# Kernel optimization log

Measured on AMD Instinct MI355X. Metric: run time of the kernel, lower is better.

Reference implementation:

```python
import jax, jax.numpy as jnp
import numpy as np


def setup_inputs() -> dict:
    key = jax.random.key(0)
    k0, k1, k2, k3 = jax.random.split(key, 4)
    B, T, D, F, E = 4, 2048, 512, 1024, 8
    x = jax.random.normal(k0, (B, T, D), dtype=jnp.float32)
    # router weight is zero-init in the original; use small random values so top-k
    router_w = 0.02 * jax.random.normal(k1, (E, D), dtype=jnp.float32)
    router_b = jnp.zeros((E,), dtype=jnp.float32)
    w_gate_up = 0.02 * jax.random.normal(k2, (E, D, 2 * F), dtype=jnp.float32)
    w_down = 0.02 * jax.random.normal(k3, (E, F, D), dtype=jnp.float32)
    return {"x": x, "router_w": router_w, "router_b": router_b,
            "w_gate_up": w_gate_up, "w_down": w_down, "top_k": 2}


def reference(x, router_w, router_b, w_gate_up, w_down, top_k):
    B, T, D = x.shape
    E = router_w.shape[0]
    x_flat = x.reshape(-1, D)                      # [N, D]
    N = x_flat.shape[0]

    # router: softmax over experts, top-k, renormalize
    logits = x_flat @ router_w.T + router_b       # [N, E]
    probs = jax.nn.softmax(logits, axis=-1)
    top_w, top_idx = jax.lax.top_k(probs, top_k)  # [N, k]
    top_w = top_w / jnp.sum(top_w, axis=-1, keepdims=True)

    # scatter renormalized weights into a dense [N, E] combine matrix
    combine = jnp.zeros((N, E), dtype=x.dtype).at[
        jnp.arange(N)[:, None], top_idx].add(top_w)

    # per-expert SwiGLU; combine weights zero out non-selected experts, giving
    # math identical to the sort/gather/scatter dispatch in the original
    out = jnp.zeros_like(x_flat)
    for e in range(E):  # fixed small expert count, not a data-dim loop
        gate_up = x_flat @ w_gate_up[e]           # [N, 2F]
        gate, up = jnp.split(gate_up, 2, axis=-1)
        h = jax.nn.silu(gate) * up                # [N, F]
        out = out + combine[:, e:e + 1] * (h @ w_down[e])
    return out.reshape(B, T, D)
```

## Files before the change

### kernel.cpp

```cpp
#include <hip/hip_runtime.h>
#include <stdint.h>

#define N_TOK 8192
#define D_DIM 512
#define F_DIM 1024
#define E_NUM 8
#define M_SLOTS (N_TOK * 2)
#define NTILE_MAX 136

typedef __bf16 bf16x8 __attribute__((ext_vector_type(8)));
typedef float f32x4 __attribute__((ext_vector_type(4)));

__device__ __forceinline__ ushort f2b(float f) {
    union { float f; unsigned u; } v; v.f = f;
    unsigned r = v.u + 0x7fffu + ((v.u >> 16) & 1u);
    return (ushort)(r >> 16);
}
__device__ __forceinline__ float b2f(ushort u) {
    union { unsigned i; float f; } v; v.i = ((unsigned)u) << 16; return v.f;
}
__device__ __forceinline__ void gload16(const void* g, void* l) {
    __builtin_amdgcn_global_load_lds(
        (const __attribute__((address_space(1))) unsigned int*)g,
        (__attribute__((address_space(3))) unsigned int*)l, 16, 0, 0);
}

__global__ __launch_bounds__(256) void pre_k(const float* __restrict__ x,
                                             const float* __restrict__ rw,
                                             const float* __restrict__ rb,
                                             ushort* __restrict__ x_bf,
                                             int* __restrict__ tok_e,
                                             float* __restrict__ tok_w,
                                             int* __restrict__ cnt,
                                             const float* __restrict__ wgu,
                                             ushort* __restrict__ wgu_t,
                                             const float* __restrict__ wd,
                                             ushort* __restrict__ wd_t) {
    __shared__ ushort tile[64][65];
    int b = blockIdx.x;
    if (b < N_TOK / 4) {
        if (b == 0 && threadIdx.x < 16) cnt[threadIdx.x] = 0;
        int lane = threadIdx.x & 63, wv = threadIdx.x >> 6;
        int t = b * 4 + wv;
        float4 xa = *(const float4*)(x + (size_t)t * D_DIM + lane * 8);
        float4 xb = *(const float4*)(x + (size_t)t * D_DIM + lane * 8 + 4);
        ushort u[8] = {f2b(xa.x), f2b(xa.y), f2b(xa.z), f2b(xa.w),
                       f2b(xb.x), f2b(xb.y), f2b(xb.z), f2b(xb.w)};
        *(uint4*)(x_bf + (size_t)t * D_DIM + lane * 8) = *(const uint4*)u;

        float acc[E_NUM];
#pragma unroll
        for (int e = 0; e < E_NUM; ++e) {
            float4 wa = *(const float4*)(rw + (size_t)e * D_DIM + lane * 8);
            float4 wb = *(const float4*)(rw + (size_t)e * D_DIM + lane * 8 + 4);
            float s = xa.x * wa.x + xa.y * wa.y + xa.z * wa.z + xa.w * wa.w +
                      xb.x * wb.x + xb.y * wb.y + xb.z * wb.z + xb.w * wb.w;
#pragma unroll
            for (int o = 32; o > 0; o >>= 1) s += __shfl_xor(s, o, 64);
            acc[e] = s;
        }
        if (lane == 0) {
            float l[E_NUM];
#pragma unroll
            for (int e = 0; e < E_NUM; ++e) l[e] = acc[e] + rb[e];
            int e0 = 0;
#pragma unroll
            for (int e = 1; e < E_NUM; ++e) if (l[e] > l[e0]) e0 = e;
            int e1 = (e0 == 0) ? 1 : 0;
#pragma unroll
            for (int e = 0; e < E_NUM; ++e) if (e != e0 && l[e] > l[e1]) e1 = e;
            float p1 = __expf(l[e1] - l[e0]);
            float w0 = 1.f / (1.f + p1), w1 = p1 / (1.f + p1);
            tok_e[2 * t] = e0;  tok_e[2 * t + 1] = e1;
            tok_w[2 * t] = w0;  tok_w[2 * t + 1] = w1;
        }
        return;
    }
    int tb = b - N_TOK / 4;
    const float* src; ushort* dst; int R, C, c0, r0;
    if (tb < 2048) {
        int e = tb >> 8, rem = tb & 255;
        R = D_DIM; C = 2 * F_DIM;
        src = wgu + (size_t)e * R * C; dst = wgu_t + (size_t)e * R * C;
        c0 = (rem & 31) * 64; r0 = (rem >> 5) * 64;
    } else {
        int b2 = tb - 2048;
        int e = b2 >> 7, rem = b2 & 127;
        R = F_DIM; C = D_DIM;
        src = wd + (size_t)e * R * C; dst = wd_t + (size_t)e * R * C;
        c0 = (rem & 7) * 64; r0 = (rem >> 3) * 64;
    }
#pragma unroll
    for (int i = 0; i < 4; ++i) {
        int ch = threadIdx.x + i * 256;
        int row = ch >> 4, pos = ch & 15;
        float4 v = *(const float4*)(src + (size_t)(r0 + row) * C + c0 + pos * 4);
        tile[row][pos * 4 + 0] = f2b(v.x);
        tile[row][pos * 4 + 1] = f2b(v.y);
        tile[row][pos * 4 + 2] = f2b(v.z);
        tile[row][pos * 4 + 3] = f2b(v.w);
    }
    __syncthreads();
#pragma unroll
    for (int i = 0; i < 2; ++i) {
        int ch = threadIdx.x + i * 256;
        int ocol = ch >> 3, rb_ = ch & 7;
        ushort tmp[8];
#pragma unroll
        for (int j = 0; j < 8; ++j) tmp[j] = tile[rb_ * 8 + j][ocol];
        *(uint4*)(dst + (size_t)(c0 + ocol) * R + r0 + rb_ * 8) = *(const uint4*)tmp;
    }
}

__global__ __launch_bounds__(256) void assign_k(const int* __restrict__ tok_e,
                                                int* __restrict__ cnt,
                                                int* __restrict__ rank) {
    __shared__ int lcnt[E_NUM], lbase[E_NUM];
    int tid = threadIdx.x;
    int i = blockIdx.x * 256 + tid;
    if (tid < E_NUM) lcnt[tid] = 0;
    __syncthreads();
    int e = tok_e[i];
    int intra = atomicAdd(&lcnt[e], 1);
    __syncthreads();
    if (tid < E_NUM) lbase[tid] = atomicAdd(&cnt[tid], lcnt[tid]);
    __syncthreads();
    rank[i] = lbase[e] + intra;
}

__global__ __launch_bounds__(256) void scatter_k(const int* __restrict__ tok_e,
                                                 const int* __restrict__ rank,
                                                 const int* __restrict__ cnt,
                                                 int* __restrict__ ebase,
                                                 int* __restrict__ row_token,
                                                 int* __restrict__ tok_pos,
                                                 int* __restrict__ tmap) {
    __shared__ int eb[E_NUM];
    int tid = threadIdx.x;
    if (tid == 0) {
        int s = 0;
        for (int k = 0; k < E_NUM; ++k) {
            eb[k] = s;
            if (blockIdx.x == 0) ebase[k] = s;
            s += cnt[k];
        }
        if (blockIdx.x == 0) {
            ebase[E_NUM] = s;
            int idx = 0;
            for (int k = 0; k < E_NUM; ++k)
                for (int t0 = 0; t0 * 128 < cnt[k]; ++t0)
                    tmap[idx++] = (k << 16) | t0;
            for (; idx < NTILE_MAX; ++idx) tmap[idx] = -1;
        }
    }
    __syncthreads();
    int i = blockIdx.x * 256 + tid;
    int pos = eb[tok_e[i]] + rank[i];
    row_token[pos] = i >> 1;
    tok_pos[i] = pos;
}

__global__ __launch_bounds__(256, 3) void gemm1_k(const ushort* __restrict__ x,
                                                  const ushort* __restrict__ wgu_t,
                                                  const int* __restrict__ ebase,
                                                  const int* __restrict__ row_token,
                                                  const int* __restrict__ tmap,
                                                  ushort* __restrict__ h) {
    int tm = tmap[blockIdx.y];
    if (tm < 0) return;
    int e = tm >> 16;
    int tile0 = (tm & 0xffff) * 128;
    int base = ebase[e];
    int cnt = ebase[e + 1] - base;
    int c0 = blockIdx.x * 64;

    __shared__ __align__(16) ushort smem[3 * 8192];

    int tid = threadIdx.x;
    int lane = tid & 63, wv = tid >> 6;
    int wr = wv >> 1, wc = wv & 1;

    const ushort* asrc[2];
    const ushort* bsrc[2];
#pragma unroll
    for (int i = 0; i < 2; ++i) {
        int c = tid + i * 256;
        int rp = c >> 3, s = c & 7;
        int lp = s ^ (rp & 7);
        int row = 2 * rp + (lp >> 2);
        int q = lp & 3;
        int r = tile0 + row;
        r = (r < cnt) ? r : (cnt - 1);
        int tok = row_token[base + r];
        asrc[i] = x + (size_t)tok * D_DIM + q * 8;
        int gc = (row < 64) ? (c0 + row) : (F_DIM + c0 + row - 64);
        bsrc[i] = wgu_t + ((size_t)e * (2 * F_DIM) + gc) * D_DIM + q * 8;
    }

    f32x4 accg[4][2], accu[4][2];
#pragma unroll
    for (int a = 0; a < 4; ++a)
#pragma unroll
        for (int b = 0; b < 2; ++b) {
            accg[a][b] = (f32x4){0.f, 0.f, 0.f, 0.f};
            accu[a][b] = (f32x4){0.f, 0.f, 0.f, 0.f};
        }

    int q = lane >> 4, m = lane & 15;
    int mh = m >> 1;
    int sl = (4 * (m & 1) + q) ^ (mh & 7);
    int soff = sl * 8;

    auto stage = [&](ushort* buf, int kk) {
#pragma unroll
        for (int i = 0; i < 2; ++i) {
            int c = tid + i * 256;
            gload16(asrc[i] + kk, buf + (size_t)c * 8);
            gload16(bsrc[i] + kk, buf + 4096 + (size_t)c * 8);
        }
    };
    auto compute = [&](const ushort* la_) {
        const ushort* lb_ = la_ + 4096;
        bf16x8 af[4], bg[2], bu[2];
#pragma unroll
        for (int mt = 0; mt < 4; ++mt)
            af[mt] = *(const bf16x8*)(la_ + (wr * 32 + mt * 8 + mh) * 64 + soff);
#pragma unroll
        for (int nt = 0; nt < 2; ++nt) {
            bg[nt] = *(const bf16x8*)(lb_ + (wc * 16 + nt * 8 + mh) * 64 + soff);
            bu[nt] = *(const bf16x8*)(lb_ + (32 + wc * 16 + nt * 8 + mh) * 64 + soff);
        }
#pragma unroll
        for (int mt = 0; mt < 4; ++mt)
#pragma unroll
            for (int nt = 0; nt < 2; ++nt) {
                accg[mt][nt] = __builtin_amdgcn_mfma_f32_16x16x32_bf16(af[mt], bg[nt], accg[mt][nt], 0, 0, 0);
                accu[mt][nt] = __builtin_amdgcn_mfma_f32_16x16x32_bf16(af[mt], bu[nt], accu[mt][nt], 0, 0, 0);
            }
    };

    ushort* pc = smem;
    ushort* pn = smem + 8192;
    ushort* pf = smem + 16384;

    stage(pc, 0);
    stage(pn, 32);
    asm volatile("s_waitcnt vmcnt(4) lgkmcnt(0)" ::: "memory");
    __builtin_amdgcn_s_barrier();
    __builtin_amdgcn_sched_barrier(0);

    for (int k = 64; k <= D_DIM - 32; k += 32) {
        stage(pf, k);
        compute(pc);
        asm volatile("s_waitcnt vmcnt(4) lgkmcnt(0)" ::: "memory");
        __builtin_amdgcn_s_barrier();
        __builtin_amdgcn_sched_barrier(0);
        ushort* t_ = pc; pc = pn; pn = pf; pf = t_;
    }
    compute(pc);
    asm volatile("s_waitcnt vmcnt(0) lgkmcnt(0)" ::: "memory");
    __builtin_amdgcn_s_barrier();
    __builtin_amdgcn_sched_barrier(0);
    compute(pn);

    __syncthreads();
    ushort* stg = smem;
#pragma unroll
    for (int mt = 0; mt < 4; ++mt)
#pragma unroll
        for (int nt = 0; nt < 2; ++nt) {
            int sc = wc * 32 + nt * 16 + m;
#pragma unroll
            for (int r4 = 0; r4 < 4; ++r4) {
                int rr = wr * 64 + mt * 16 + q * 4 + r4;
                float g = accg[mt][nt][r4];
                float u = accu[mt][nt][r4];
                stg[rr * 68 + sc] = f2b((g / (1.f + __expf(-g))) * u);
            }
        }
    __syncthreads();
#pragma unroll
    for (int p = 0; p < 4; ++p) {
        int c = tid + p * 256;
        int sr = c >> 3, coff = (c & 7) * 8;
        int grow = tile0 + sr;
        if (grow < cnt)
            *(uint4*)(h + (size_t)(base + grow) * F_DIM + c0 + coff) =
                *(const uint4*)(stg + sr * 68 + coff);
    }
}

__global__ __launch_bounds__(256, 3) void gemm2_k(const ushort* __restrict__ h,
                                                  const ushort* __restrict__ wd_t,
                                                  const int* __restrict__ ebase,
                                                  const int* __restrict__ tmap,
                                                  ushort* __restrict__ slot) {
    int tm = tmap[blockIdx.y];
    if (tm < 0) return;
    int e = tm >> 16;
    int tile0 = (tm & 0xffff) * 128;
    int base = ebase[e];
    int cnt = ebase[e + 1] - base;
    int c0 = blockIdx.x * 128;

    __shared__ __align__(16) ushort smem[3 * 8192];

    int tid = threadIdx.x;
    int lane = tid & 63, wv = tid >> 6;
    int wr = wv >> 1, wc = wv & 1;

    const ushort* asrc[2]; const ushort* bsrc[2];
#pragma unroll
    for (int i = 0; i < 2; ++i) {
        int c = tid + i * 256;
        int rp = c >> 3, s = c & 7;
        int lp = s ^ (rp & 7);
        int row = 2 * rp + (lp >> 2);
        int q = lp & 3;
        int r = tile0 + row;
        r = (r < cnt) ? r : (cnt - 1);
        asrc[i] = h + (size_t)(base + r) * F_DIM + q * 8;
        bsrc[i] = wd_t + ((size_t)e * D_DIM + c0 + row) * F_DIM + q * 8;
    }

    f32x4 acc[4][4];
#pragma unroll
    for (int a = 0; a < 4; ++a)
#pragma unroll
        for (int b = 0; b < 4; ++b) acc[a][b] = (f32x4){0.f, 0.f, 0.f, 0.f};

    int q = lane >> 4, m = lane & 15;
    int mh = m >> 1;
    int sl = (4 * (m & 1) + q) ^ (mh & 7);
    int soff = sl * 8;

    auto stage = [&](ushort* buf, int kk) {
#pragma unroll
        for (int i = 0; i < 2; ++i) {
            int c = tid + i * 256;
            gload16(asrc[i] + kk, buf + (size_t)c * 8);
            gload16(bsrc[i] + kk, buf + 4096 + (size_t)c * 8);
        }
    };
    auto compute = [&](const ushort* la_) {
        const ushort* lb_ = la_ + 4096;
        bf16x8 af[4], bb[4];
#pragma unroll
        for (int mt = 0; mt < 4; ++mt)
            af[mt] = *(const bf16x8*)(la_ + (wr * 32 + mt * 8 + mh) * 64 + soff);
#pragma unroll
        for (int nt = 0; nt < 4; ++nt)
            bb[nt] = *(const bf16x8*)(lb_ + (wc * 32 + nt * 8 + mh) * 64 + soff);
        __builtin_amdgcn_s_setprio(1);
#pragma unroll
        for (int mt = 0; mt < 4; ++mt)
#pragma unroll
            for (int nt = 0; nt < 4; ++nt)
                acc[mt][nt] = __builtin_amdgcn_mfma_f32_16x16x32_bf16(af[mt], bb[nt], acc[mt][nt], 0, 0, 0);
        __builtin_amdgcn_s_setprio(0);
    };

    ushort* pc = smem;
    ushort* pn = smem + 8192;
    ushort* pf = smem + 16384;

    stage(pc, 0);
    stage(pn, 32);
    asm volatile("s_waitcnt vmcnt(4) lgkmcnt(0)" ::: "memory");
    __builtin_amdgcn_s_barrier();
    __builtin_amdgcn_sched_barrier(0);

    for (int k = 64; k <= F_DIM - 32; k += 32) {
        stage(pf, k);
        compute(pc);
        asm volatile("s_waitcnt vmcnt(4) lgkmcnt(0)" ::: "memory");
        __builtin_amdgcn_s_barrier();
        __builtin_amdgcn_sched_barrier(0);
        ushort* t_ = pc; pc = pn; pn = pf; pf = t_;
    }
    compute(pc);
    asm volatile("s_waitcnt vmcnt(0) lgkmcnt(0)" ::: "memory");
    __builtin_amdgcn_s_barrier();
    __builtin_amdgcn_sched_barrier(0);
    compute(pn);

    __syncthreads();
    ushort* stg = smem;
#pragma unroll
    for (int mt = 0; mt < 4; ++mt)
#pragma unroll
        for (int nt = 0; nt < 4; ++nt) {
            int scol = wc * 64 + nt * 16 + m;
#pragma unroll
            for (int r4 = 0; r4 < 4; ++r4) {
                int rr = wr * 64 + mt * 16 + q * 4 + r4;
                stg[rr * 132 + scol] = f2b(acc[mt][nt][r4]);
            }
        }
    __syncthreads();
#pragma unroll
    for (int p = 0; p < 8; ++p) {
        int c = tid + p * 256;
        int sr = c >> 4, coff = (c & 15) * 8;
        int grow = tile0 + sr;
        if (grow < cnt)
            *(uint4*)(slot + (size_t)(base + grow) * D_DIM + c0 + coff) =
                *(const uint4*)(stg + sr * 132 + coff);
    }
}

__global__ __launch_bounds__(256) void combine_k(const ushort* __restrict__ slot,
                                                 const int* __restrict__ tok_pos,
                                                 const float* __restrict__ tok_w,
                                                 float* __restrict__ out) {
    int lane = threadIdx.x & 63, wv = threadIdx.x >> 6;
    int t = blockIdx.x * 4 + wv;
    int p0 = tok_pos[2 * t], p1 = tok_pos[2 * t + 1];
    float w0 = tok_w[2 * t], w1 = tok_w[2 * t + 1];
    uint4 s0 = *(const uint4*)(slot + (size_t)p0 * D_DIM + lane * 8);
    uint4 s1 = *(const uint4*)(slot + (size_t)p1 * D_DIM + lane * 8);
    const ushort* a = (const ushort*)&s0;
    const ushort* b = (const ushort*)&s1;
    float o[8];
#pragma unroll
    for (int j = 0; j < 8; ++j) o[j] = w0 * b2f(a[j]) + w1 * b2f(b[j]);
    float* dst = out + (size_t)t * D_DIM + lane * 8;
    *(float4*)dst = (float4){o[0], o[1], o[2], o[3]};
    *(float4*)(dst + 4) = (float4){o[4], o[5], o[6], o[7]};
}

extern "C" void kernel_launch(void* const* d_in, const int* in_sizes, int n_in,
                              void* d_out, int out_size, void* d_ws, size_t ws_size,
                              hipStream_t stream) {
    const float* x   = (const float*)d_in[0];
    const float* rw  = (const float*)d_in[1];
    const float* rb  = (const float*)d_in[2];
    const float* wgu = (const float*)d_in[3];
    const float* wd  = (const float*)d_in[4];
    float* out = (float*)d_out;

    char* ws = (char*)d_ws;
    size_t off = 0;
    auto alloc = [&](size_t bytes) -> void* {
        void* p = ws + off;
        off += (bytes + 255) & ~(size_t)255;
        return p;
    };
    ushort* wgu_t     = (ushort*)alloc((size_t)E_NUM * 2 * F_DIM * D_DIM * 2);
    ushort* wd_t      = (ushort*)alloc((size_t)E_NUM * D_DIM * F_DIM * 2);
    ushort* x_bf      = (ushort*)alloc((size_t)N_TOK * D_DIM * 2);
    ushort* hbuf      = (ushort*)alloc((size_t)M_SLOTS * F_DIM * 2);
    ushort* slot      = (ushort*)alloc((size_t)M_SLOTS * D_DIM * 2);
    int*    row_token = (int*)alloc(M_SLOTS * 4);
    int*    tok_e     = (int*)alloc(M_SLOTS * 4);
    int*    rankbuf   = (int*)alloc(M_SLOTS * 4);
    float*  tok_w     = (float*)alloc(M_SLOTS * 4);
    int*    tok_pos   = (int*)alloc(M_SLOTS * 4);
    int*    cnt       = (int*)alloc(64);
    int*    ebase     = (int*)alloc(64);
    int*    tmap      = (int*)alloc(NTILE_MAX * 4);

    pre_k<<<N_TOK / 4 + 3072, 256, 0, stream>>>(x, rw, rb, x_bf, tok_e, tok_w, cnt,
                                                wgu, wgu_t, wd, wd_t);
    assign_k<<<M_SLOTS / 256, 256, 0, stream>>>(tok_e, cnt, rankbuf);
    scatter_k<<<M_SLOTS / 256, 256, 0, stream>>>(tok_e, rankbuf, cnt, ebase,
                                                 row_token, tok_pos, tmap);
    gemm1_k<<<dim3(16, NTILE_MAX), 256, 0, stream>>>(x_bf, wgu_t, ebase, row_token, tmap, hbuf);
    gemm2_k<<<dim3(4, NTILE_MAX), 256, 0, stream>>>(hbuf, wd_t, ebase, tmap, slot);
    combine_k<<<N_TOK / 4, 256, 0, stream>>>(slot, tok_pos, tok_w, out);
}
```

Baseline: 206.5 us.

## Enlarge gemm1 row tile to 256 with 512-thread blocks and separate tile map

The first expert GEMM now uses 256-row tiles handled by 512-thread blocks of 8 waves, so each staged weight tile feeds twice as many token rows. scatter_k builds a second tile map for 256-row tiles, while gemm2 keeps the 128-row map. The aim is to halve redundant weight loads and raise arithmetic intensity per block. The cost is a larger shared-memory footprint, fewer blocks, and more padding waste on the partial last tile of each expert.

```diff
diff --git a/kernel.cpp b/kernel.cpp
--- a/kernel.cpp
+++ b/kernel.cpp
@@ -6,7 +6,8 @@
 #define F_DIM 1024
 #define E_NUM 8
 #define M_SLOTS (N_TOK * 2)
-#define NTILE_MAX 136
+#define NT128_MAX 136
+#define NT256_MAX 72
 
 typedef __bf16 bf16x8 __attribute__((ext_vector_type(8)));
 typedef float f32x4 __attribute__((ext_vector_type(4)));
@@ -134,7 +135,8 @@
                                                  int* __restrict__ ebase,
                                                  int* __restrict__ row_token,
                                                  int* __restrict__ tok_pos,
-                                                 int* __restrict__ tmap) {
+                                                 int* __restrict__ tmap128,
+                                                 int* __restrict__ tmap256) {
     __shared__ int eb[E_NUM];
     int tid = threadIdx.x;
     if (tid == 0) {
@@ -146,11 +148,13 @@
         }
         if (blockIdx.x == 0) {
             ebase[E_NUM] = s;
-            int idx = 0;
-            for (int k = 0; k < E_NUM; ++k)
-                for (int t0 = 0; t0 * 128 < cnt[k]; ++t0)
-                    tmap[idx++] = (k << 16) | t0;
-            for (; idx < NTILE_MAX; ++idx) tmap[idx] = -1;
+            int i1 = 0, i2 = 0;
+            for (int k = 0; k < E_NUM; ++k) {
+                for (int t0 = 0; t0 * 128 < cnt[k]; ++t0) tmap128[i1++] = (k << 16) | t0;
+                for (int t0 = 0; t0 * 256 < cnt[k]; ++t0) tmap256[i2++] = (k << 16) | t0;
+            }
+            for (; i1 < NT128_MAX; ++i1) tmap128[i1] = -1;
+            for (; i2 < NT256_MAX; ++i2) tmap256[i2] = -1;
         }
     }
     __syncthreads();
@@ -160,7 +164,7 @@
     tok_pos[i] = pos;
 }
 
-__global__ __launch_bounds__(256, 3) void gemm1_k(const ushort* __restrict__ x,
+__global__ __launch_bounds__(512, 4) void gemm1_k(const ushort* __restrict__ x,
                                                   const ushort* __restrict__ wgu_t,
                                                   const int* __restrict__ ebase,
                                                   const int* __restrict__ row_token,
@@ -169,32 +173,35 @@
     int tm = tmap[blockIdx.y];
     if (tm < 0) return;
     int e = tm >> 16;
-    int tile0 = (tm & 0xffff) * 128;
+    int tile0 = (tm & 0xffff) * 256;
     int base = ebase[e];
     int cnt = ebase[e + 1] - base;
     int c0 = blockIdx.x * 64;
 
-    __shared__ __align__(16) ushort smem[3 * 8192];
+    __shared__ __align__(16) ushort smem[3 * 12288];
 
     int tid = threadIdx.x;
     int lane = tid & 63, wv = tid >> 6;
     int wr = wv >> 1, wc = wv & 1;
 
-    const ushort* asrc[2];
-    const ushort* bsrc[2];
-#pragma unroll
-    for (int i = 0; i < 2; ++i) {
-        int c = tid + i * 256;
+    const ushort* src3[3];
+#pragma unroll
+    for (int i = 0; i < 3; ++i) {
+        int c6 = tid + i * 512;
+        int c = (c6 < 1024) ? c6 : (c6 - 1024);
         int rp = c >> 3, s = c & 7;
         int lp = s ^ (rp & 7);
         int row = 2 * rp + (lp >> 2);
         int q = lp & 3;
-        int r = tile0 + row;
-        r = (r < cnt) ? r : (cnt - 1);
-        int tok = row_token[base + r];
-        asrc[i] = x + (size_t)tok * D_DIM + q * 8;
-        int gc = (row < 64) ? (c0 + row) : (F_DIM + c0 + row - 64);
-        bsrc[i] = wgu_t + ((size_t)e * (2 * F_DIM) + gc) * D_DIM + q * 8;
+        if (c6 < 1024) {
+            int r = tile0 + row;
+            r = (r < cnt) ? r : (cnt - 1);
+            int tok = row_token[base + r];
+            src3[i] = x + (size_t)tok * D_DIM + q * 8;
+        } else {
+            int gc = (row < 64) ? (c0 + row) : (F_DIM + c0 + row - 64);
+            src3[i] = wgu_t + ((size_t)e * (2 * F_DIM) + gc) * D_DIM + q * 8;
+        }
     }
 
     f32x4 accg[4][2], accu[4][2];
@@ -213,14 +220,13 @@
 
     auto stage = [&](ushort* buf, int kk) {
 #pragma unroll
-        for (int i = 0; i < 2; ++i) {
-            int c = tid + i * 256;
-            gload16(asrc[i] + kk, buf + (size_t)c * 8);
-            gload16(bsrc[i] + kk, buf + 4096 + (size_t)c * 8);
+        for (int i = 0; i < 3; ++i) {
+            int c6 = tid + i * 512;
+            gload16(src3[i] + kk, buf + (size_t)c6 * 8);
         }
     };
     auto compute = [&](const ushort* la_) {
-        const ushort* lb_ = la_ + 4096;
+        const ushort* lb_ = la_ + 8192;
         bf16x8 af[4], bg[2], bu[2];
 #pragma unroll
         for (int mt = 0; mt < 4; ++mt)
@@ -240,19 +246,19 @@
     };
 
     ushort* pc = smem;
-    ushort* pn = smem + 8192;
-    ushort* pf = smem + 16384;
+    ushort* pn = smem + 12288;
+    ushort* pf = smem + 24576;
 
     stage(pc, 0);
     stage(pn, 32);
-    asm volatile("s_waitcnt vmcnt(4) lgkmcnt(0)" ::: "memory");
+    asm volatile("s_waitcnt vmcnt(3) lgkmcnt(0)" ::: "memory");
     __builtin_amdgcn_s_barrier();
     __builtin_amdgcn_sched_barrier(0);
 
     for (int k = 64; k <= D_DIM - 32; k += 32) {
         stage(pf, k);
         compute(pc);
-        asm volatile("s_waitcnt vmcnt(4) lgkmcnt(0)" ::: "memory");
+        asm volatile("s_waitcnt vmcnt(3) lgkmcnt(0)" ::: "memory");
         __builtin_amdgcn_s_barrier();
         __builtin_amdgcn_sched_barrier(0);
         ushort* t_ = pc; pc = pn; pn = pf; pf = t_;
@@ -281,7 +287,7 @@
     __syncthreads();
 #pragma unroll
     for (int p = 0; p < 4; ++p) {
-        int c = tid + p * 256;
+        int c = tid + p * 512;
         int sr = c >> 3, coff = (c & 7) * 8;
         int grow = tile0 + sr;
         if (grow < cnt)
@@ -458,14 +464,15 @@
     int*    tok_pos   = (int*)alloc(M_SLOTS * 4);
     int*    cnt       = (int*)alloc(64);
     int*    ebase     = (int*)alloc(64);
-    int*    tmap      = (int*)alloc(NTILE_MAX * 4);
+    int*    tmap128   = (int*)alloc(NT128_MAX * 4);
+    int*    tmap256   = (int*)alloc(NT256_MAX * 4);
 
     pre_k<<<N_TOK / 4 + 3072, 256, 0, stream>>>(x, rw, rb, x_bf, tok_e, tok_w, cnt,
                                                 wgu, wgu_t, wd, wd_t);
     assign_k<<<M_SLOTS / 256, 256, 0, stream>>>(tok_e, cnt, rankbuf);
     scatter_k<<<M_SLOTS / 256, 256, 0, stream>>>(tok_e, rankbuf, cnt, ebase,
-                                                 row_token, tok_pos, tmap);
-    gemm1_k<<<dim3(16, NTILE_MAX), 256, 0, stream>>>(x_bf, wgu_t, ebase, row_token, tmap, hbuf);
-    gemm2_k<<<dim3(4, NTILE_MAX), 256, 0, stream>>>(hbuf, wd_t, ebase, tmap, slot);
+                                                 row_token, tok_pos, tmap128, tmap256);
+    gemm1_k<<<dim3(16, NT256_MAX), 512, 0, stream>>>(x_bf, wgu_t, ebase, row_token, tmap256, hbuf);
+    gemm2_k<<<dim3(4, NT128_MAX), 256, 0, stream>>>(hbuf, wd_t, ebase, tmap128, slot);
     combine_k<<<N_TOK / 4, 256, 0, stream>>>(slot, tok_pos, tok_w, out);
 }
```

New measurement: 208.0 us. About the same (+0.7%).
